# Optimization experiments

Measured on AMD Instinct MI355X. Metric: run time of the kernel, lower is better.

The kernel has to match this reference:

```python
import jax, jax.numpy as jnp
import numpy as np

B, LAGS, POOL, D, H, NTS = 16, 4096, 4, 512, 8, 1000
S = LAGS // POOL          # num_pools = 1024
DH = D // H               # head dim = 64


def _layernorm_dim1(x, gamma, beta, eps=1e-5):
    # torch code: mean/var over dim=1 (channel axis), unbiased var, per-position affine
    mean = jnp.mean(x, axis=1, keepdims=True)
    var = jnp.var(x, axis=1, keepdims=True, ddof=1)
    unit = (x - mean) / jnp.sqrt(eps + var)
    return gamma * unit + beta


def setup_inputs() -> dict:
    key = jax.random.key(0)
    ks = jax.random.split(key, 16)
    inp = {
        "ts": jax.random.normal(ks[0], (B, 1, LAGS), dtype=jnp.float32),
        "te": jax.random.randint(ks[1], (B, 1), 0, NTS),
        "conv_w": jax.random.normal(ks[2], (D, 1, POOL), dtype=jnp.float32) * (1.0 / POOL) ** 0.5,
        "conv_b": jax.random.normal(ks[3], (D,), dtype=jnp.float32) * 0.02,
        "pe_emb": jax.random.normal(ks[4], (S, D), dtype=jnp.float32),
        "ts_emb": jax.random.normal(ks[5], (NTS, D), dtype=jnp.float32),
        "ln1_g": jnp.ones((S,), dtype=jnp.float32),
        "ln1_b": jnp.zeros((S,), dtype=jnp.float32),
        "dense_M": jax.random.normal(ks[6], (D, D), dtype=jnp.float32) * D ** -0.5,
        "Wq": jax.random.normal(ks[7], (H, DH, D), dtype=jnp.float32) * D ** -0.5,
        "Wk": jax.random.normal(ks[8], (H, DH, D), dtype=jnp.float32) * D ** -0.5,
        "Wv": jax.random.normal(ks[9], (H, DH, D), dtype=jnp.float32) * D ** -0.5,
        "Wo": jax.random.normal(ks[10], (D, D), dtype=jnp.float32) * D ** -0.5,
        "bo": jnp.zeros((D, 1), dtype=jnp.float32),
        "ln2_g": jnp.ones((S,), dtype=jnp.float32),
        "ln2_b": jnp.zeros((S,), dtype=jnp.float32),
    }
    return inp


def _forward(ts, te, conv_w, conv_b, pe_emb, ts_emb, ln1_g, ln1_b,
             dense_M, Wq, Wk, Wv, Wo, bo, ln2_g, ln2_b):
    # Conv1d with stride == kernel_size: non-overlapping patches
    xr = ts.reshape(B, S, POOL)                                   # (B,S,P)
    conv = jnp.einsum('bsp,dp->bds', xr, conv_w[:, 0, :]) + conv_b[:, None]  # (B,D,S)
    conv = conv + pe_emb.T                                        # positional add (D,S)
    act = jax.nn.gelu(conv, approximate=False)
    n1 = _layernorm_dim1(act, ln1_g, ln1_b)
    dense = jnp.einsum('ed,bds->bes', dense_M, n1)                # Linear: M @ x
    dense = dense + ts_emb[te[:, 0]][:, :, None]                  # ts embedding (B,D,1)

    # multi-head attention, Q=K=V=dense; vectorized over heads
    Qd = jnp.einsum('hcd,bds->bhcs', Wq, dense)                   # (B,H,DH,S)
    Kd = jnp.einsum('hcd,bds->bhcs', Wk, dense)
    Vd = jnp.einsum('hcd,bds->bhcs', Wv, dense)
    scores = jnp.einsum('bhci,bhcj->bhij', Qd, Kd) / DH ** 0.5    # (B,H,S,S)
    i_idx = jnp.arange(S)
    mask = i_idx[:, None] > i_idx[None, :]                        # tril(diagonal=-1): i>j -> -inf
    scores = jnp.where(mask, -jnp.inf, scores)
    sm = jax.nn.softmax(scores, axis=2)                           # softmax over dim 1 of (S,S)
    attn = jnp.einsum('bhci,bhij->bhcj', Vd, sm)                  # V @ softmaxed
    cat = attn.reshape(B, D, S)                                   # concat heads on dim 1
    out = jnp.einsum('ed,bds->bes', Wo, cat) + bo[None]           # final linear + bias
    res = out + conv                                              # residual
    return _layernorm_dim1(res, ln2_g, ln2_b)


def reference(ts, te, conv_w, conv_b, pe_emb, ts_emb, ln1_g, ln1_b,
              dense_M, Wq, Wk, Wv, Wo, bo, ln2_g, ln2_b):
    return _forward(ts, te, conv_w, conv_b, pe_emb, ts_emb, ln1_g, ln1_b,
                    dense_M, Wq, Wk, Wv, Wo, bo, ln2_g, ln2_b)
```

## Files before the change

### kernel.cpp

```cpp
#include <hip/hip_runtime.h>
#include <hip/hip_bf16.h>

#define B_ 16
#define S_ 1024
#define D_ 512
#define H_ 8
#define DH_ 64

typedef __attribute__((ext_vector_type(8))) short bf16x8;
typedef __attribute__((ext_vector_type(4))) short bf16x4;
typedef __attribute__((ext_vector_type(4))) float f32x4;
typedef __attribute__((ext_vector_type(16))) float f32x16;

__device__ __forceinline__ short f2bf(float f) {
    __hip_bfloat16 h = __float2bfloat16(f);
    return *reinterpret_cast<short*>(&h);
}
__device__ __forceinline__ float bf2f(short s) {
    unsigned u = ((unsigned)(unsigned short)s) << 16;
    return __uint_as_float(u);
}
__device__ __forceinline__ unsigned pack_bf2(float lo, float hi) {
    unsigned a = (unsigned)(unsigned short)f2bf(lo);
    unsigned b = (unsigned)(unsigned short)f2bf(hi);
    return a | (b << 16);
}
__device__ __forceinline__ void gload16(const void* g, void* l) {
    __builtin_amdgcn_global_load_lds(
        (const __attribute__((address_space(1))) unsigned int*)g,
        (__attribute__((address_space(3))) unsigned int*)l, 16, 0, 0);
}

__global__ __launch_bounds__(256) void prep_w(
    const float* __restrict__ M, const float* __restrict__ Wq,
    const float* __restrict__ Wk, const float* __restrict__ Wv,
    const float* __restrict__ Wo, __hip_bfloat16* __restrict__ wb)
{
    __hip_bfloat16* wsrc = wb;
    __hip_bfloat16* Wob  = wb + 786432;
    __hip_bfloat16* MT   = wb + 1048576;

    const int blk = blockIdx.x, t = threadIdx.x;
    if (blk < 512) {
        const int wi = blk >> 7;
        const int off = (blk & 127) * 2048 + t * 8;
        const float* src = (wi == 0) ? Wq : (wi == 1) ? Wk : (wi == 2) ? Wv : Wo;
        const float scale = (wi == 0) ? 0.18033688011112042f : 1.0f;
        const float4 f0 = *reinterpret_cast<const float4*>(src + off);
        const float4 f1 = *reinterpret_cast<const float4*>(src + off + 4);
        const float fv[8] = {f0.x, f0.y, f0.z, f0.w, f1.x, f1.y, f1.z, f1.w};
        union { short s[8]; bf16x8 v; } r;
#pragma unroll
        for (int j = 0; j < 8; ++j) r.s[j] = f2bf(fv[j] * scale);
        __hip_bfloat16* dst = (wi == 3) ? (Wob + off) : (wsrc + wi * 262144 + off);
        *reinterpret_cast<bf16x8*>(dst) = r.v;
    } else {
        __shared__ float tile[32][33];
        const int tt = blk - 512;
        const int e0 = (tt & 15) * 32, d0 = (tt >> 4) * 32;
        const int r = t >> 5, c = t & 31;
#pragma unroll
        for (int k = 0; k < 4; ++k)
            tile[r + k * 8][c] = M[(size_t)(e0 + r + k * 8) * 512 + d0 + c];
        __syncthreads();
#pragma unroll
        for (int k = 0; k < 4; ++k)
            MT[(size_t)(d0 + r + k * 8) * 512 + e0 + c] =
                __float2bfloat16(tile[c][r + k * 8]);
    }
}

__global__ __launch_bounds__(256) void bias_k(
    const __hip_bfloat16* __restrict__ wsrc, const float* __restrict__ ts_emb,
    const int* __restrict__ te, float* __restrict__ qkvpart)
{
    const int blk = blockIdx.x;
    const int w16b = blk >> 2, dc = blk & 3;
    const int b = w16b & 15, w = w16b >> 4;
    const float* e = ts_emb + (size_t)te[b] * 512 + dc * 128;
#pragma unroll
    for (int rep = 0; rep < 2; ++rep) {
        const int n = threadIdx.x + rep * 256;
        const __hip_bfloat16* wr = wsrc + ((size_t)(w * 512 + n)) * 512 + dc * 128;
        float s = 0.f;
#pragma unroll 4
        for (int d8 = 0; d8 < 128; d8 += 8) {
            const bf16x8 wv8 = *reinterpret_cast<const bf16x8*>(wr + d8);
            const float4 e0 = *reinterpret_cast<const float4*>(e + d8);
            const float4 e1 = *reinterpret_cast<const float4*>(e + d8 + 4);
            s += bf2f(wv8[0]) * e0.x + bf2f(wv8[1]) * e0.y
               + bf2f(wv8[2]) * e0.z + bf2f(wv8[3]) * e0.w
               + bf2f(wv8[4]) * e1.x + bf2f(wv8[5]) * e1.y
               + bf2f(wv8[6]) * e1.z + bf2f(wv8[7]) * e1.w;
        }
        qkvpart[(size_t)dc * 24576 + (size_t)w16b * 512 + n] = s;
    }
}

__global__ __launch_bounds__(256) void k1_conv_gelu_ln(
    const float* __restrict__ ts, const float* __restrict__ conv_w,
    const float* __restrict__ conv_b, const float* __restrict__ pe,
    const float* __restrict__ g1, const float* __restrict__ b1,
    __hip_bfloat16* __restrict__ n1)
{
    const int w = threadIdx.x >> 6, lane = threadIdx.x & 63;
    const int row = blockIdx.x * 4 + w;
    const int b = row >> 10, s = row & 1023;
    const float4 x = *reinterpret_cast<const float4*>(ts + b * 4096 + s * 4);
    const int d0 = lane * 8;

    const float4 cb0 = *reinterpret_cast<const float4*>(conv_b + d0);
    const float4 cb1 = *reinterpret_cast<const float4*>(conv_b + d0 + 4);
    const float4 pe0 = *reinterpret_cast<const float4*>(pe + s * 512 + d0);
    const float4 pe1 = *reinterpret_cast<const float4*>(pe + s * 512 + d0 + 4);
    const float cbv[8] = {cb0.x, cb0.y, cb0.z, cb0.w, cb1.x, cb1.y, cb1.z, cb1.w};
    const float pev[8] = {pe0.x, pe0.y, pe0.z, pe0.w, pe1.x, pe1.y, pe1.z, pe1.w};

    float a[8];
    float sum = 0.f, sq = 0.f;
#pragma unroll
    for (int j = 0; j < 8; ++j) {
        const float4 wv = *reinterpret_cast<const float4*>(conv_w + (d0 + j) * 4);
        float v = x.x * wv.x + x.y * wv.y + x.z * wv.z + x.w * wv.w
                + cbv[j] + pev[j];
        v = 0.5f * v * (1.0f + erff(v * 0.70710678118654752f));
        a[j] = v; sum += v; sq += v * v;
    }
#pragma unroll
    for (int off = 1; off < 64; off <<= 1) {
        sum += __shfl_xor(sum, off);
        sq  += __shfl_xor(sq, off);
    }
    const float mean = sum * (1.0f / 512.0f);
    const float var  = (sq - 512.0f * mean * mean) * (1.0f / 511.0f);
    const float rstd = rsqrtf(var + 1e-5f);
    const float gg = g1[s], bb = b1[s];
    union { short sh[8]; bf16x8 v; } o;
#pragma unroll
    for (int j = 0; j < 8; ++j)
        o.sh[j] = f2bf(gg * ((a[j] - mean) * rstd) + bb);
    *reinterpret_cast<bf16x8*>(n1 + (size_t)row * 512 + d0) = o.v;
}

template<int MODE>
__global__ __launch_bounds__(256, 2) void gemm_k(
    const __hip_bfloat16* __restrict__ A,
    const __hip_bfloat16* __restrict__ Wb,
    void* __restrict__ outp,
    const float* __restrict__ aux)
{
    __shared__ char lA[2][128 * 128];
    __shared__ char lB[2][128 * 128];

    const int t = threadIdx.x;
    const int lane = t & 63;
    const int w = t >> 6;
    const int wm = w & 1, wn = w >> 1;
    const int Rb = blockIdx.x * 128;
    const int Nb = blockIdx.y * 128;
    const int g = lane >> 4, lr = lane & 15;
    const int lrow = lane >> 3;
    const int coff = ((lane & 7) ^ lrow) * 8;

    const __hip_bfloat16* asrc = A  + (size_t)(Rb + lrow) * 512 + coff;
    const __hip_bfloat16* bsrc = Wb + (size_t)(Nb + lrow) * 512 + coff;

    f32x4 acc[4][4];
#pragma unroll
    for (int i = 0; i < 4; ++i)
#pragma unroll
        for (int j = 0; j < 4; ++j) acc[i][j] = {0.f, 0.f, 0.f, 0.f};

    auto stage = [&](int buf, int k0) {
#pragma unroll
        for (int i = 0; i < 4; ++i) {
            const int r0 = w * 32 + i * 8;
            gload16(asrc + (size_t)r0 * 512 + k0, &lA[buf][r0 * 128]);
        }
#pragma unroll
        for (int i = 0; i < 4; ++i) {
            const int r0 = w * 32 + i * 8;
            gload16(bsrc + (size_t)r0 * 512 + k0, &lB[buf][r0 * 128]);
        }
    };

    stage(0, 0);
    __syncthreads();

    for (int kt = 0; kt < 8; ++kt) {
        const int buf = kt & 1;
        if (kt < 7) stage(buf ^ 1, (kt + 1) * 64);
#pragma unroll
        for (int kk = 0; kk < 2; ++kk) {
            bf16x8 af[4], bfv[4];
            const int ch = kk * 4 + g;
#pragma unroll
            for (int mt = 0; mt < 4; ++mt) {
                const int row = wm * 64 + mt * 16 + lr;
                af[mt] = *reinterpret_cast<const bf16x8*>(
                    &lA[buf][row * 128 + ((ch ^ (row & 7)) << 4)]);
            }
#pragma unroll
            for (int nt = 0; nt < 4; ++nt) {
                const int row = wn * 64 + nt * 16 + lr;
                bfv[nt] = *reinterpret_cast<const bf16x8*>(
                    &lB[buf][row * 128 + ((ch ^ (row & 7)) << 4)]);
            }
#pragma unroll
            for (int mt = 0; mt < 4; ++mt)
#pragma unroll
                for (int nt = 0; nt < 4; ++nt)
                    acc[mt][nt] = __builtin_amdgcn_mfma_f32_16x16x32_bf16(
                        af[mt], bfv[nt], acc[mt][nt], 0, 0, 0);
        }
        __syncthreads();
    }

    const int w3 = Nb >> 9;
#pragma unroll
    for (int mt = 0; mt < 4; ++mt) {
#pragma unroll
        for (int nt = 0; nt < 4; ++nt) {
#pragma unroll
            for (int r = 0; r < 4; ++r) {
                const int R = Rb + wm * 64 + mt * 16 + 4 * g + r;
                const int N = Nb + wn * 64 + nt * 16 + lr;
                float v = acc[mt][nt][r];
                if (MODE == 5) {
                    const int Nl = N & 511;
                    const int b = R >> 10, s = R & 1023, h = Nl >> 6, c = Nl & 63;
                    const float* qp = aux + (size_t)(w3 * 16 + b) * 512 + Nl;
                    v += qp[0] + qp[24576] + qp[49152] + qp[73728];
                    __hip_bfloat16* base =
                        reinterpret_cast<__hip_bfloat16*>(outp) + (size_t)w3 * 8388608;
                    if (w3 == 2)
                        base[(((size_t)(b * 8 + h)) * 64 + c) * 1024 + s] =
                            __float2bfloat16(v);
                    else
                        base[(((size_t)(b * 8 + h)) * 1024 + s) * 64 + c] =
                            __float2bfloat16(v);
                } else if (MODE == 6) {
                    reinterpret_cast<__hip_bfloat16*>(outp)[(size_t)R * 512 + N] =
                        __float2bfloat16(v);
                } else {
                    reinterpret_cast<float*>(outp)[(size_t)R * 512 + N] = v + aux[N];
                }
            }
        }
    }
}

__device__ __forceinline__ void write_strip(
    __hip_bfloat16* __restrict__ dstbase, const int jw0,
    const f32x16& o0, const f32x16& o1, const float lsum,
    const int l5, const int ln31)
{
    const float linv = 1.0f / lsum;
#pragma unroll
    for (int r = 0; r < 16; ++r) {
        const int jrow = (r & 3) + 8 * (r >> 2) + 4 * l5;
        const float rinv = __shfl(linv, jrow);
        __hip_bfloat16* dst = dstbase + (size_t)(jw0 + jrow) * 512;
        dst[ln31]      = __float2bfloat16(o0[r] * rinv);
        dst[32 + ln31] = __float2bfloat16(o1[r] * rinv);
    }
}

__global__ __launch_bounds__(256, 4) void attn5_k(
    const __hip_bfloat16* __restrict__ Qm,
    const __hip_bfloat16* __restrict__ Km,
    const __hip_bfloat16* __restrict__ Vt,
    __hip_bfloat16* __restrict__ cat)
{
    __shared__ char qbuf[2][4096];
    __shared__ char vbuf[2][4096];

    const int t = threadIdx.x, lane = t & 63, w = t >> 6;
    const int l5 = lane >> 5, ln31 = lane & 31;
    const int id = blockIdx.x;
    const int bh = id & 127;
    const int jb = (0x32451067u >> ((id >> 7) * 4)) & 7;
    const int b = bh >> 3, h = bh & 7;
    const int j0 = jb * 128 + w * 32;

    const __hip_bfloat16* Qh = Qm + (size_t)bh * (S_ * 64);
    const __hip_bfloat16* Kh = Km + (size_t)bh * (S_ * 64);
    const __hip_bfloat16* Vh = Vt + (size_t)bh * (64 * S_);

    bf16x8 kf[4];
#pragma unroll
    for (int kt = 0; kt < 4; ++kt)
        kf[kt] = *reinterpret_cast<const bf16x8*>(
            Kh + (size_t)(j0 + ln31) * 64 + kt * 16 + l5 * 8);

    f32x16 o0, o1;
#pragma unroll
    for (int r = 0; r < 16; ++r) { o0[r] = 0.f; o1[r] = 0.f; }
    float m = -3e38f, lsum = 0.f;

    const int last = jb * 4 + w;
    const int ntiles = jb * 4 + 4;

    const int q_row  = w * 8 + (lane >> 3);
    const int q_ch   = (lane & 7) ^ (lane >> 3);
    const int v_row  = w * 16 + (lane >> 2);
    const int v_ch   = (lane & 3) ^ ((lane >> 2) & 3) ^ ((lane >> 4) & 3);
    const __hip_bfloat16* qsrc = Qh + (size_t)q_row * 64 + q_ch * 8;
    const __hip_bfloat16* vsrc = Vh + (size_t)v_row * 1024 + v_ch * 8;

    auto stage = [&](int buf, int tile) {
        const int i0 = tile * 32;
        gload16(qsrc + (size_t)i0 * 64, &qbuf[buf][w * 1024]);
        gload16(vsrc + i0,              &vbuf[buf][w * 1024]);
    };

    stage(0, 0);
    __syncthreads();

    for (int tt = 0; tt < ntiles; ++tt) {
        const int buf = tt & 1;
        if (tt + 1 < ntiles) stage(buf ^ 1, tt + 1);
        if (tt <= last) {
            f32x16 sc;
#pragma unroll
            for (int r = 0; r < 16; ++r) sc[r] = 0.f;
            bf16x8 qf[4];
#pragma unroll
            for (int kt = 0; kt < 4; ++kt)
                qf[kt] = *reinterpret_cast<const bf16x8*>(
                    &qbuf[buf][ln31 * 128 + (((kt * 2 + l5) ^ (ln31 & 7)) << 4)]);
#pragma unroll
            for (int kt = 0; kt < 4; ++kt)
                sc = __builtin_amdgcn_mfma_f32_32x32x16_bf16(qf[kt], kf[kt], sc, 0, 0, 0);

            union u8 { bf16x4 h[2]; bf16x8 v; };
            u8 vf[2][2];
#pragma unroll
            for (int kt = 0; kt < 2; ++kt) {
#pragma unroll
                for (int dh = 0; dh < 2; ++dh) {
                    const int drow = ln31 + dh * 32;
                    const int swz = (drow & 3) ^ ((drow >> 2) & 3);
                    const int x0 = kt * 32 + 8 * l5;
#pragma unroll
                    for (int hp = 0; hp < 2; ++hp) {
                        const int x = x0 + hp * 16;
                        vf[kt][dh].h[hp] = *reinterpret_cast<const bf16x4*>(
                            &vbuf[buf][drow * 64 + (((x >> 4) ^ swz) << 4) + (x & 15)]);
                    }
                }
            }

            const bool diag = (tt == last);
            float p[16];
            float mx = -3e38f;
            if (diag) {
#pragma unroll
                for (int r = 0; r < 16; ++r) {
                    const int irow = (r & 3) + 8 * (r >> 2) + 4 * l5;
                    const float v = (irow > ln31) ? -3e38f : sc[r];
                    p[r] = v; mx = fmaxf(mx, v);
                }
            } else {
#pragma unroll
                for (int r = 0; r < 16; ++r) { p[r] = sc[r]; mx = fmaxf(mx, sc[r]); }
            }
            mx = fmaxf(mx, __shfl_xor(mx, 32));
            if (!__all(mx <= m + 8.0f)) {
                const float mn = fmaxf(m, mx);
                const float alpha = exp2f(m - mn);
                m = mn; lsum *= alpha;
#pragma unroll
                for (int r = 0; r < 16; ++r) {
                    const int jrow = (r & 3) + 8 * (r >> 2) + 4 * l5;
                    const float ar = __shfl(alpha, jrow);
                    o0[r] *= ar; o1[r] *= ar;
                }
            }
            float ps = 0.f;
#pragma unroll
            for (int r = 0; r < 16; ++r) { p[r] = exp2f(p[r] - m); ps += p[r]; }
            ps += __shfl_xor(ps, 32);
            lsum += ps;

            union { unsigned u[4]; bf16x8 v; } pa0, pa1;
            pa0.u[0] = pack_bf2(p[0],  p[1]);  pa0.u[1] = pack_bf2(p[2],  p[3]);
            pa0.u[2] = pack_bf2(p[4],  p[5]);  pa0.u[3] = pack_bf2(p[6],  p[7]);
            pa1.u[0] = pack_bf2(p[8],  p[9]);  pa1.u[1] = pack_bf2(p[10], p[11]);
            pa1.u[2] = pack_bf2(p[12], p[13]); pa1.u[3] = pack_bf2(p[14], p[15]);
            o0 = __builtin_amdgcn_mfma_f32_32x32x16_bf16(pa0.v, vf[0][0].v, o0, 0, 0, 0);
            o1 = __builtin_amdgcn_mfma_f32_32x32x16_bf16(pa0.v, vf[0][1].v, o1, 0, 0, 0);
            o0 = __builtin_amdgcn_mfma_f32_32x32x16_bf16(pa1.v, vf[1][0].v, o0, 0, 0, 0);
            o1 = __builtin_amdgcn_mfma_f32_32x32x16_bf16(pa1.v, vf[1][1].v, o1, 0, 0, 0);
        }
        __syncthreads();
    }

    __hip_bfloat16* dstbase = cat + (size_t)b * 1024 * 512 + h * 64;
    write_strip(dstbase, j0, o0, o1, lsum, l5, ln31);
}

__global__ __launch_bounds__(256) void k5_res_ln(
    const float* __restrict__ outf,
    const float* __restrict__ ts, const float* __restrict__ conv_w,
    const float* __restrict__ conv_b, const float* __restrict__ pe,
    const float* __restrict__ g2, const float* __restrict__ b2,
    float* __restrict__ out)
{
    __shared__ float tile[16 * 520];
    const int blk = blockIdx.x;
    const int b = blk >> 6, s0 = (blk & 63) * 16;
    const int t = threadIdx.x;
    const int sl = t >> 4, c = t & 15;
    const int s = s0 + sl;

    const float4 x = *reinterpret_cast<const float4*>(ts + b * 4096 + s * 4);
    float vals[32];
    float sum = 0.f, sq = 0.f;
#pragma unroll
    for (int j = 0; j < 32; ++j) {
        const int d = c + 16 * j;
        const float4 wv = *reinterpret_cast<const float4*>(conv_w + d * 4);
        const float conv = x.x * wv.x + x.y * wv.y + x.z * wv.z + x.w * wv.w
                         + conv_b[d] + pe[s * 512 + d];
        const float a = outf[(size_t)(b * 1024 + s) * 512 + d] + conv;
        vals[j] = a; sum += a; sq += a * a;
    }
#pragma unroll
    for (int off = 1; off < 16; off <<= 1) {
        sum += __shfl_xor(sum, off);
        sq  += __shfl_xor(sq, off);
    }
    const float mean = sum * (1.0f / 512.0f);
    const float var  = (sq - 512.0f * mean * mean) * (1.0f / 511.0f);
    const float rstd = rsqrtf(var + 1e-5f);
    const float gg = g2[s], bb = b2[s];
#pragma unroll
    for (int j = 0; j < 32; ++j) {
        const int d = c + 16 * j;
        tile[sl * 520 + d] = gg * ((vals[j] - mean) * rstd) + bb;
    }
    __syncthreads();
#pragma unroll
    for (int q2 = 0; q2 < 2; ++q2) {
        const int d = t + q2 * 256;
        float buf[16];
#pragma unroll
        for (int sl2 = 0; sl2 < 16; ++sl2) buf[sl2] = tile[sl2 * 520 + d];
        float4* dst = reinterpret_cast<float4*>(
            out + ((size_t)b * 512 + d) * 1024 + s0);
        dst[0] = make_float4(buf[0],  buf[1],  buf[2],  buf[3]);
        dst[1] = make_float4(buf[4],  buf[5],  buf[6],  buf[7]);
        dst[2] = make_float4(buf[8],  buf[9],  buf[10], buf[11]);
        dst[3] = make_float4(buf[12], buf[13], buf[14], buf[15]);
    }
}

extern "C" void kernel_launch(void* const* d_in, const int* in_sizes, int n_in,
                              void* d_out, int out_size, void* d_ws, size_t ws_size,
                              hipStream_t stream)
{
    const float* ts     = (const float*)d_in[0];
    const int*   te     = (const int*)d_in[1];
    const float* conv_w = (const float*)d_in[2];
    const float* conv_b = (const float*)d_in[3];
    const float* pe     = (const float*)d_in[4];
    const float* ts_emb = (const float*)d_in[5];
    const float* g1     = (const float*)d_in[6];
    const float* b1     = (const float*)d_in[7];
    const float* M      = (const float*)d_in[8];
    const float* Wq     = (const float*)d_in[9];
    const float* Wk     = (const float*)d_in[10];
    const float* Wv     = (const float*)d_in[11];
    const float* Wo     = (const float*)d_in[12];
    const float* bo     = (const float*)d_in[13];
    const float* g2     = (const float*)d_in[14];
    const float* b2     = (const float*)d_in[15];

    char* ws = (char*)d_ws;
    __hip_bfloat16* wb     = (__hip_bfloat16*)(ws);
    __hip_bfloat16* wsrc   = wb;
    __hip_bfloat16* Wob    = wb + 786432;
    __hip_bfloat16* MT     = wb + 1048576;
    __hip_bfloat16* Wqkvp  = (__hip_bfloat16*)(ws + (2688ull << 10));
    float*          qkvpart= (float*)(ws + (4608ull << 10));
    __hip_bfloat16* n1     = (__hip_bfloat16*)(ws + ( 6ull << 20));
    __hip_bfloat16* cat    = n1;
    __hip_bfloat16* q      = (__hip_bfloat16*)(ws + (22ull << 20));
    __hip_bfloat16* k      = (__hip_bfloat16*)(ws + (38ull << 20));
    __hip_bfloat16* vT     = (__hip_bfloat16*)(ws + (54ull << 20));
    float*          outf   = (float*)(ws + (22ull << 20));

    prep_w<<<768, 256, 0, stream>>>(M, Wq, Wk, Wv, Wo, wb);
    bias_k<<<192, 256, 0, stream>>>(wsrc, ts_emb, te, qkvpart);
    gemm_k<6><<<dim3(12, 4), 256, 0, stream>>>(wsrc, MT, Wqkvp, nullptr);
    k1_conv_gelu_ln<<<4096, 256, 0, stream>>>(ts, conv_w, conv_b, pe, g1, b1, n1);
    gemm_k<5><<<dim3(128, 12), 256, 0, stream>>>(n1, Wqkvp, q, qkvpart);
    attn5_k<<<1024, 256, 0, stream>>>(q, k, vT, cat);
    gemm_k<3><<<dim3(128, 4), 256, 0, stream>>>(cat, Wob, outf, bo);
    k5_res_ln<<<1024, 256, 0, stream>>>(outf, ts, conv_w, conv_b, pe, g2, b2,
                                        (float*)d_out);
}
```

Before: 174.3 us.

## Merge front kernels, pair causal attention blocks, store output projection in bf16

Fuses weight prep, bias computation and conv/GELU/LayerNorm into one launch, and the bias path now reads fp32 weights directly. The attention kernel has each block process two complementary causal strips (jb and 7-jb), so the grid is half as large and per-block work is even. The output projection writes bf16 instead of fp32, which halves that intermediate's traffic. The cost is lower precision in the residual input and less occupancy in attention, since the launch bound drops to 2 blocks.

Result: slower. 196.0 us (+12.5%).

```diff
diff --git a/kernel.cpp b/kernel.cpp
--- a/kernel.cpp
+++ b/kernel.cpp
@@ -31,115 +31,106 @@
         (__attribute__((address_space(3))) unsigned int*)l, 16, 0, 0);
 }
 
-__global__ __launch_bounds__(256) void prep_w(
-    const float* __restrict__ M, const float* __restrict__ Wq,
-    const float* __restrict__ Wk, const float* __restrict__ Wv,
-    const float* __restrict__ Wo, __hip_bfloat16* __restrict__ wb)
-{
-    __hip_bfloat16* wsrc = wb;
-    __hip_bfloat16* Wob  = wb + 786432;
-    __hip_bfloat16* MT   = wb + 1048576;
-
-    const int blk = blockIdx.x, t = threadIdx.x;
-    if (blk < 512) {
-        const int wi = blk >> 7;
-        const int off = (blk & 127) * 2048 + t * 8;
-        const float* src = (wi == 0) ? Wq : (wi == 1) ? Wk : (wi == 2) ? Wv : Wo;
-        const float scale = (wi == 0) ? 0.18033688011112042f : 1.0f;
-        const float4 f0 = *reinterpret_cast<const float4*>(src + off);
-        const float4 f1 = *reinterpret_cast<const float4*>(src + off + 4);
-        const float fv[8] = {f0.x, f0.y, f0.z, f0.w, f1.x, f1.y, f1.z, f1.w};
-        union { short s[8]; bf16x8 v; } r;
-#pragma unroll
-        for (int j = 0; j < 8; ++j) r.s[j] = f2bf(fv[j] * scale);
-        __hip_bfloat16* dst = (wi == 3) ? (Wob + off) : (wsrc + wi * 262144 + off);
-        *reinterpret_cast<bf16x8*>(dst) = r.v;
-    } else {
-        __shared__ float tile[32][33];
-        const int tt = blk - 512;
-        const int e0 = (tt & 15) * 32, d0 = (tt >> 4) * 32;
-        const int r = t >> 5, c = t & 31;
-#pragma unroll
-        for (int k = 0; k < 4; ++k)
-            tile[r + k * 8][c] = M[(size_t)(e0 + r + k * 8) * 512 + d0 + c];
-        __syncthreads();
-#pragma unroll
-        for (int k = 0; k < 4; ++k)
-            MT[(size_t)(d0 + r + k * 8) * 512 + e0 + c] =
-                __float2bfloat16(tile[c][r + k * 8]);
-    }
-}
-
-__global__ __launch_bounds__(256) void bias_k(
-    const __hip_bfloat16* __restrict__ wsrc, const float* __restrict__ ts_emb,
-    const int* __restrict__ te, float* __restrict__ qkvpart)
-{
-    const int blk = blockIdx.x;
-    const int w16b = blk >> 2, dc = blk & 3;
-    const int b = w16b & 15, w = w16b >> 4;
-    const float* e = ts_emb + (size_t)te[b] * 512 + dc * 128;
-#pragma unroll
-    for (int rep = 0; rep < 2; ++rep) {
-        const int n = threadIdx.x + rep * 256;
-        const __hip_bfloat16* wr = wsrc + ((size_t)(w * 512 + n)) * 512 + dc * 128;
-        float s = 0.f;
-#pragma unroll 4
-        for (int d8 = 0; d8 < 128; d8 += 8) {
-            const bf16x8 wv8 = *reinterpret_cast<const bf16x8*>(wr + d8);
-            const float4 e0 = *reinterpret_cast<const float4*>(e + d8);
-            const float4 e1 = *reinterpret_cast<const float4*>(e + d8 + 4);
-            s += bf2f(wv8[0]) * e0.x + bf2f(wv8[1]) * e0.y
-               + bf2f(wv8[2]) * e0.z + bf2f(wv8[3]) * e0.w
-               + bf2f(wv8[4]) * e1.x + bf2f(wv8[5]) * e1.y
-               + bf2f(wv8[6]) * e1.z + bf2f(wv8[7]) * e1.w;
-        }
-        qkvpart[(size_t)dc * 24576 + (size_t)w16b * 512 + n] = s;
-    }
-}
-
-__global__ __launch_bounds__(256) void k1_conv_gelu_ln(
+__global__ __launch_bounds__(256) void front_k(
     const float* __restrict__ ts, const float* __restrict__ conv_w,
     const float* __restrict__ conv_b, const float* __restrict__ pe,
     const float* __restrict__ g1, const float* __restrict__ b1,
-    __hip_bfloat16* __restrict__ n1)
-{
-    const int w = threadIdx.x >> 6, lane = threadIdx.x & 63;
-    const int row = blockIdx.x * 4 + w;
-    const int b = row >> 10, s = row & 1023;
-    const float4 x = *reinterpret_cast<const float4*>(ts + b * 4096 + s * 4);
-    const int d0 = lane * 8;
-
-    const float4 cb0 = *reinterpret_cast<const float4*>(conv_b + d0);
-    const float4 cb1 = *reinterpret_cast<const float4*>(conv_b + d0 + 4);
-    const float4 pe0 = *reinterpret_cast<const float4*>(pe + s * 512 + d0);
-    const float4 pe1 = *reinterpret_cast<const float4*>(pe + s * 512 + d0 + 4);
-    const float cbv[8] = {cb0.x, cb0.y, cb0.z, cb0.w, cb1.x, cb1.y, cb1.z, cb1.w};
-    const float pev[8] = {pe0.x, pe0.y, pe0.z, pe0.w, pe1.x, pe1.y, pe1.z, pe1.w};
-
-    float a[8];
-    float sum = 0.f, sq = 0.f;
-#pragma unroll
-    for (int j = 0; j < 8; ++j) {
-        const float4 wv = *reinterpret_cast<const float4*>(conv_w + (d0 + j) * 4);
-        float v = x.x * wv.x + x.y * wv.y + x.z * wv.z + x.w * wv.w
-                + cbv[j] + pev[j];
-        v = 0.5f * v * (1.0f + erff(v * 0.70710678118654752f));
-        a[j] = v; sum += v; sq += v * v;
-    }
-#pragma unroll
-    for (int off = 1; off < 64; off <<= 1) {
-        sum += __shfl_xor(sum, off);
-        sq  += __shfl_xor(sq, off);
-    }
-    const float mean = sum * (1.0f / 512.0f);
-    const float var  = (sq - 512.0f * mean * mean) * (1.0f / 511.0f);
-    const float rstd = rsqrtf(var + 1e-5f);
-    const float gg = g1[s], bb = b1[s];
-    union { short sh[8]; bf16x8 v; } o;
-#pragma unroll
-    for (int j = 0; j < 8; ++j)
-        o.sh[j] = f2bf(gg * ((a[j] - mean) * rstd) + bb);
-    *reinterpret_cast<bf16x8*>(n1 + (size_t)row * 512 + d0) = o.v;
+    const float* __restrict__ M, const float* __restrict__ Wq,
+    const float* __restrict__ Wk, const float* __restrict__ Wv,
+    const float* __restrict__ Wo, const float* __restrict__ ts_emb,
+    const int* __restrict__ te,
+    __hip_bfloat16* __restrict__ n1, __hip_bfloat16* __restrict__ wb,
+    float* __restrict__ qkvpart)
+{
+    const int blk = blockIdx.x, t = threadIdx.x;
+    if (blk < 4096) {
+        const int w = t >> 6, lane = t & 63;
+        const int row = blk * 4 + w;
+        const int b = row >> 10, s = row & 1023;
+        const float4 x = *reinterpret_cast<const float4*>(ts + b * 4096 + s * 4);
+        const int d0 = lane * 8;
+        const float4 cb0 = *reinterpret_cast<const float4*>(conv_b + d0);
+        const float4 cb1 = *reinterpret_cast<const float4*>(conv_b + d0 + 4);
+        const float4 pe0 = *reinterpret_cast<const float4*>(pe + s * 512 + d0);
+        const float4 pe1 = *reinterpret_cast<const float4*>(pe + s * 512 + d0 + 4);
+        const float cbv[8] = {cb0.x, cb0.y, cb0.z, cb0.w, cb1.x, cb1.y, cb1.z, cb1.w};
+        const float pev[8] = {pe0.x, pe0.y, pe0.z, pe0.w, pe1.x, pe1.y, pe1.z, pe1.w};
+        float a[8];
+        float sum = 0.f, sq = 0.f;
+#pragma unroll
+        for (int j = 0; j < 8; ++j) {
+            const float4 wv = *reinterpret_cast<const float4*>(conv_w + (d0 + j) * 4);
+            float v = x.x * wv.x + x.y * wv.y + x.z * wv.z + x.w * wv.w
+                    + cbv[j] + pev[j];
+            v = 0.5f * v * (1.0f + erff(v * 0.70710678118654752f));
+            a[j] = v; sum += v; sq += v * v;
+        }
+#pragma unroll
+        for (int off = 1; off < 64; off <<= 1) {
+            sum += __shfl_xor(sum, off);
+            sq  += __shfl_xor(sq, off);
+        }
+        const float mean = sum * (1.0f / 512.0f);
+        const float var  = (sq - 512.0f * mean * mean) * (1.0f / 511.0f);
+        const float rstd = rsqrtf(var + 1e-5f);
+        const float gg = g1[s], bb = b1[s];
+        union { short sh[8]; bf16x8 v; } o;
+#pragma unroll
+        for (int j = 0; j < 8; ++j)
+            o.sh[j] = f2bf(gg * ((a[j] - mean) * rstd) + bb);
+        *reinterpret_cast<bf16x8*>(n1 + (size_t)row * 512 + d0) = o.v;
+    } else if (blk < 4864) {
+        __hip_bfloat16* wsrc = wb;
+        __hip_bfloat16* Wob  = wb + 786432;
+        __hip_bfloat16* MT   = wb + 1048576;
+        const int pblk = blk - 4096;
+        if (pblk < 512) {
+            const int wi = pblk >> 7;
+            const int off = (pblk & 127) * 2048 + t * 8;
+            const float* src = (wi == 0) ? Wq : (wi == 1) ? Wk : (wi == 2) ? Wv : Wo;
+            const float scale = (wi == 0) ? 0.18033688011112042f : 1.0f;
+            const float4 f0 = *reinterpret_cast<const float4*>(src + off);
+            const float4 f1 = *reinterpret_cast<const float4*>(src + off + 4);
+            const float fv[8] = {f0.x, f0.y, f0.z, f0.w, f1.x, f1.y, f1.z, f1.w};
+            union { short s[8]; bf16x8 v; } r;
+#pragma unroll
+            for (int j = 0; j < 8; ++j) r.s[j] = f2bf(fv[j] * scale);
+            __hip_bfloat16* dst = (wi == 3) ? (Wob + off) : (wsrc + wi * 262144 + off);
+            *reinterpret_cast<bf16x8*>(dst) = r.v;
+        } else {
+            __shared__ float tile[32][33];
+            const int tt = pblk - 512;
+            const int e0 = (tt & 15) * 32, d0 = (tt >> 4) * 32;
+            const int r = t >> 5, c = t & 31;
+#pragma unroll
+            for (int k = 0; k < 4; ++k)
+                tile[r + k * 8][c] = M[(size_t)(e0 + r + k * 8) * 512 + d0 + c];
+            __syncthreads();
+#pragma unroll
+            for (int k = 0; k < 4; ++k)
+                MT[(size_t)(d0 + r + k * 8) * 512 + e0 + c] =
+                    __float2bfloat16(tile[c][r + k * 8]);
+        }
+    } else {
+        const int bblk = blk - 4864;
+        const int w16b = bblk >> 2, dc = bblk & 3;
+        const int b = w16b & 15, w = w16b >> 4;
+        const float* W = (w == 0) ? Wq : (w == 1) ? Wk : Wv;
+        const float scale = (w == 0) ? 0.18033688011112042f : 1.0f;
+        const float* e = ts_emb + (size_t)te[b] * 512 + dc * 128;
+#pragma unroll
+        for (int rep = 0; rep < 2; ++rep) {
+            const int n = t + rep * 256;
+            const float* wr = W + (size_t)n * 512 + dc * 128;
+            float s = 0.f;
+            for (int d = 0; d < 128; d += 4) {
+                const float4 a = *reinterpret_cast<const float4*>(wr + d);
+                const float4 bb = *reinterpret_cast<const float4*>(e + d);
+                s += a.x * bb.x + a.y * bb.y + a.z * bb.z + a.w * bb.w;
+            }
+            qkvpart[(size_t)dc * 24576 + (size_t)w16b * 512 + n] = s * scale;
+        }
+    }
 }
 
 template<int MODE>
@@ -243,7 +234,8 @@
                     reinterpret_cast<__hip_bfloat16*>(outp)[(size_t)R * 512 + N] =
                         __float2bfloat16(v);
                 } else {
-                    reinterpret_cast<float*>(outp)[(size_t)R * 512 + N] = v + aux[N];
+                    reinterpret_cast<__hip_bfloat16*>(outp)[(size_t)R * 512 + N] =
+                        __float2bfloat16(v + aux[N]);
                 }
             }
         }
@@ -266,7 +258,7 @@
     }
 }
 
-__global__ __launch_bounds__(256, 4) void attn5_k(
+__global__ __launch_bounds__(256, 2) void attn6_k(
     const __hip_bfloat16* __restrict__ Qm,
     const __hip_bfloat16* __restrict__ Km,
     const __hip_bfloat16* __restrict__ Vt,
@@ -279,27 +271,12 @@
     const int l5 = lane >> 5, ln31 = lane & 31;
     const int id = blockIdx.x;
     const int bh = id & 127;
-    const int jb = (0x32451067u >> ((id >> 7) * 4)) & 7;
+    const int sidx = id >> 7;
     const int b = bh >> 3, h = bh & 7;
-    const int j0 = jb * 128 + w * 32;
 
     const __hip_bfloat16* Qh = Qm + (size_t)bh * (S_ * 64);
     const __hip_bfloat16* Kh = Km + (size_t)bh * (S_ * 64);
     const __hip_bfloat16* Vh = Vt + (size_t)bh * (64 * S_);
-
-    bf16x8 kf[4];
-#pragma unroll
-    for (int kt = 0; kt < 4; ++kt)
-        kf[kt] = *reinterpret_cast<const bf16x8*>(
-            Kh + (size_t)(j0 + ln31) * 64 + kt * 16 + l5 * 8);
-
-    f32x16 o0, o1;
-#pragma unroll
-    for (int r = 0; r < 16; ++r) { o0[r] = 0.f; o1[r] = 0.f; }
-    float m = -3e38f, lsum = 0.f;
-
-    const int last = jb * 4 + w;
-    const int ntiles = jb * 4 + 4;
 
     const int q_row  = w * 8 + (lane >> 3);
     const int q_ch   = (lane & 7) ^ (lane >> 3);
@@ -307,6 +284,7 @@
     const int v_ch   = (lane & 3) ^ ((lane >> 2) & 3) ^ ((lane >> 4) & 3);
     const __hip_bfloat16* qsrc = Qh + (size_t)q_row * 64 + q_ch * 8;
     const __hip_bfloat16* vsrc = Vh + (size_t)v_row * 1024 + v_ch * 8;
+    __hip_bfloat16* dstbase = cat + (size_t)b * 1024 * 512 + h * 64;
 
     auto stage = [&](int buf, int tile) {
         const int i0 = tile * 32;
@@ -314,94 +292,112 @@
         gload16(vsrc + i0,              &vbuf[buf][w * 1024]);
     };
 
-    stage(0, 0);
-    __syncthreads();
-
-    for (int tt = 0; tt < ntiles; ++tt) {
-        const int buf = tt & 1;
-        if (tt + 1 < ntiles) stage(buf ^ 1, tt + 1);
-        if (tt <= last) {
-            f32x16 sc;
-#pragma unroll
-            for (int r = 0; r < 16; ++r) sc[r] = 0.f;
-            bf16x8 qf[4];
-#pragma unroll
-            for (int kt = 0; kt < 4; ++kt)
-                qf[kt] = *reinterpret_cast<const bf16x8*>(
-                    &qbuf[buf][ln31 * 128 + (((kt * 2 + l5) ^ (ln31 & 7)) << 4)]);
-#pragma unroll
-            for (int kt = 0; kt < 4; ++kt)
-                sc = __builtin_amdgcn_mfma_f32_32x32x16_bf16(qf[kt], kf[kt], sc, 0, 0, 0);
-
-            union u8 { bf16x4 h[2]; bf16x8 v; };
-            u8 vf[2][2];
-#pragma unroll
-            for (int kt = 0; kt < 2; ++kt) {
-#pragma unroll
-                for (int dh = 0; dh < 2; ++dh) {
-                    const int drow = ln31 + dh * 32;
-                    const int swz = (drow & 3) ^ ((drow >> 2) & 3);
-                    const int x0 = kt * 32 + 8 * l5;
-#pragma unroll
-                    for (int hp = 0; hp < 2; ++hp) {
-                        const int x = x0 + hp * 16;
-                        vf[kt][dh].h[hp] = *reinterpret_cast<const bf16x4*>(
-                            &vbuf[buf][drow * 64 + (((x >> 4) ^ swz) << 4) + (x & 15)]);
+    for (int ph = 0; ph < 2; ++ph) {
+        const int jb = ph ? (7 - sidx) : sidx;
+        const int j0 = jb * 128 + w * 32;
+
+        bf16x8 kf[4];
+#pragma unroll
+        for (int kt = 0; kt < 4; ++kt)
+            kf[kt] = *reinterpret_cast<const bf16x8*>(
+                Kh + (size_t)(j0 + ln31) * 64 + kt * 16 + l5 * 8);
+
+        f32x16 o0, o1;
+#pragma unroll
+        for (int r = 0; r < 16; ++r) { o0[r] = 0.f; o1[r] = 0.f; }
+        float m = -3e38f, lsum = 0.f;
+
+        const int last = jb * 4 + w;
+        const int ntiles = jb * 4 + 4;
+
+        stage(0, 0);
+        __syncthreads();
+
+        for (int tt = 0; tt < ntiles; ++tt) {
+            const int buf = tt & 1;
+            if (tt + 1 < ntiles) stage(buf ^ 1, tt + 1);
+            if (tt <= last) {
+                f32x16 sc;
+#pragma unroll
+                for (int r = 0; r < 16; ++r) sc[r] = 0.f;
+                bf16x8 qf[4];
+#pragma unroll
+                for (int kt = 0; kt < 4; ++kt)
+                    qf[kt] = *reinterpret_cast<const bf16x8*>(
+                        &qbuf[buf][ln31 * 128 + (((kt * 2 + l5) ^ (ln31 & 7)) << 4)]);
+#pragma unroll
+                for (int kt = 0; kt < 4; ++kt)
+                    sc = __builtin_amdgcn_mfma_f32_32x32x16_bf16(qf[kt], kf[kt], sc, 0, 0, 0);
+
+                union u8 { bf16x4 h[2]; bf16x8 v; };
+                u8 vf[2][2];
+#pragma unroll
+                for (int kt = 0; kt < 2; ++kt) {
+#pragma unroll
+                    for (int dh = 0; dh < 2; ++dh) {
+                        const int drow = ln31 + dh * 32;
+                        const int swz = (drow & 3) ^ ((drow >> 2) & 3);
+                        const int x0 = kt * 32 + 8 * l5;
+#pragma unroll
+                        for (int hp = 0; hp < 2; ++hp) {
+                            const int x = x0 + hp * 16;
+                            vf[kt][dh].h[hp] = *reinterpret_cast<const bf16x4*>(
+                                &vbuf[buf][drow * 64 + (((x >> 4) ^ swz) << 4) + (x & 15)]);
+                        }
                     }
                 }
+
+                const bool diag = (tt == last);
+                float p[16];
+                float mx = -3e38f;
+                if (diag) {
+#pragma unroll
+                    for (int r = 0; r < 16; ++r) {
+                        const int irow = (r & 3) + 8 * (r >> 2) + 4 * l5;
+                        const float v = (irow > ln31) ? -3e38f : sc[r];
+                        p[r] = v; mx = fmaxf(mx, v);
+                    }
+                } else {
+#pragma unroll
+                    for (int r = 0; r < 16; ++r) { p[r] = sc[r]; mx = fmaxf(mx, sc[r]); }
+                }
+                mx = fmaxf(mx, __shfl_xor(mx, 32));
+                if (!__all(mx <= m + 8.0f)) {
+                    const float mn = fmaxf(m, mx);
+                    const float alpha = exp2f(m - mn);
+                    m = mn; lsum *= alpha;
+#pragma unroll
+                    for (int r = 0; r < 16; ++r) {
+                        const int jrow = (r & 3) + 8 * (r >> 2) + 4 * l5;
+                        const float ar = __shfl(alpha, jrow);
+                        o0[r] *= ar; o1[r] *= ar;
+                    }
+                }
+                float ps = 0.f;
+#pragma unroll
+                for (int r = 0; r < 16; ++r) { p[r] = exp2f(p[r] - m); ps += p[r]; }
+                ps += __shfl_xor(ps, 32);
+                lsum += ps;
+
+                union { unsigned u[4]; bf16x8 v; } pa0, pa1;
+                pa0.u[0] = pack_bf2(p[0],  p[1]);  pa0.u[1] = pack_bf2(p[2],  p[3]);
+                pa0.u[2] = pack_bf2(p[4],  p[5]);  pa0.u[3] = pack_bf2(p[6],  p[7]);
+                pa1.u[0] = pack_bf2(p[8],  p[9]);  pa1.u[1] = pack_bf2(p[10], p[11]);
+                pa1.u[2] = pack_bf2(p[12], p[13]); pa1.u[3] = pack_bf2(p[14], p[15]);
+                o0 = __builtin_amdgcn_mfma_f32_32x32x16_bf16(pa0.v, vf[0][0].v, o0, 0, 0, 0);
+                o1 = __builtin_amdgcn_mfma_f32_32x32x16_bf16(pa0.v, vf[0][1].v, o1, 0, 0, 0);
+                o0 = __builtin_amdgcn_mfma_f32_32x32x16_bf16(pa1.v, vf[1][0].v, o0, 0, 0, 0);
+                o1 = __builtin_amdgcn_mfma_f32_32x32x16_bf16(pa1.v, vf[1][1].v, o1, 0, 0, 0);
             }
-
-            const bool diag = (tt == last);
-            float p[16];
-            float mx = -3e38f;
-            if (diag) {
-#pragma unroll
-                for (int r = 0; r < 16; ++r) {
-                    const int irow = (r & 3) + 8 * (r >> 2) + 4 * l5;
-                    const float v = (irow > ln31) ? -3e38f : sc[r];
-                    p[r] = v; mx = fmaxf(mx, v);
-                }
-            } else {
-#pragma unroll
-                for (int r = 0; r < 16; ++r) { p[r] = sc[r]; mx = fmaxf(mx, sc[r]); }
-            }
-            mx = fmaxf(mx, __shfl_xor(mx, 32));
-            if (!__all(mx <= m + 8.0f)) {
-                const float mn = fmaxf(m, mx);
-                const float alpha = exp2f(m - mn);
-                m = mn; lsum *= alpha;
-#pragma unroll
-                for (int r = 0; r < 16; ++r) {
-                    const int jrow = (r & 3) + 8 * (r >> 2) + 4 * l5;
-                    const float ar = __shfl(alpha, jrow);
-                    o0[r] *= ar; o1[r] *= ar;
-                }
-            }
-            float ps = 0.f;
-#pragma unroll
-            for (int r = 0; r < 16; ++r) { p[r] = exp2f(p[r] - m); ps += p[r]; }
-            ps += __shfl_xor(ps, 32);
-            lsum += ps;
-
-            union { unsigned u[4]; bf16x8 v; } pa0, pa1;
-            pa0.u[0] = pack_bf2(p[0],  p[1]);  pa0.u[1] = pack_bf2(p[2],  p[3]);
-            pa0.u[2] = pack_bf2(p[4],  p[5]);  pa0.u[3] = pack_bf2(p[6],  p[7]);
-            pa1.u[0] = pack_bf2(p[8],  p[9]);  pa1.u[1] = pack_bf2(p[10], p[11]);
-            pa1.u[2] = pack_bf2(p[12], p[13]); pa1.u[3] = pack_bf2(p[14], p[15]);
-            o0 = __builtin_amdgcn_mfma_f32_32x32x16_bf16(pa0.v, vf[0][0].v, o0, 0, 0, 0);
-            o1 = __builtin_amdgcn_mfma_f32_32x32x16_bf16(pa0.v, vf[0][1].v, o1, 0, 0, 0);
-            o0 = __builtin_amdgcn_mfma_f32_32x32x16_bf16(pa1.v, vf[1][0].v, o0, 0, 0, 0);
-            o1 = __builtin_amdgcn_mfma_f32_32x32x16_bf16(pa1.v, vf[1][1].v, o1, 0, 0, 0);
-        }
-        __syncthreads();
-    }
-
-    __hip_bfloat16* dstbase = cat + (size_t)b * 1024 * 512 + h * 64;
-    write_strip(dstbase, j0, o0, o1, lsum, l5, ln31);
+            __syncthreads();
+        }
+
+        write_strip(dstbase, j0, o0, o1, lsum, l5, ln31);
+    }
 }
 
 __global__ __launch_bounds__(256) void k5_res_ln(
-    const float* __restrict__ outf,
+    const __hip_bfloat16* __restrict__ outf,
     const float* __restrict__ ts, const float* __restrict__ conv_w,
     const float* __restrict__ conv_b, const float* __restrict__ pe,
     const float* __restrict__ g2, const float* __restrict__ b2,
@@ -423,7 +419,7 @@
         const float4 wv = *reinterpret_cast<const float4*>(conv_w + d * 4);
         const float conv = x.x * wv.x + x.y * wv.y + x.z * wv.z + x.w * wv.w
                          + conv_b[d] + pe[s * 512 + d];
-        const float a = outf[(size_t)(b * 1024 + s) * 512 + d] + conv;
+        const float a = __bfloat162float(outf[(size_t)(b * 1024 + s) * 512 + d]) + conv;
         vals[j] = a; sum += a; sq += a * a;
     }
 #pragma unroll
@@ -489,14 +485,14 @@
     __hip_bfloat16* q      = (__hip_bfloat16*)(ws + (22ull << 20));
     __hip_bfloat16* k      = (__hip_bfloat16*)(ws + (38ull << 20));
     __hip_bfloat16* vT     = (__hip_bfloat16*)(ws + (54ull << 20));
-    float*          outf   = (float*)(ws + (22ull << 20));
-
-    prep_w<<<768, 256, 0, stream>>>(M, Wq, Wk, Wv, Wo, wb);
-    bias_k<<<192, 256, 0, stream>>>(wsrc, ts_emb, te, qkvpart);
+    __hip_bfloat16* outf   = (__hip_bfloat16*)(ws + (22ull << 20));
+
+    front_k<<<5056, 256, 0, stream>>>(ts, conv_w, conv_b, pe, g1, b1,
+                                      M, Wq, Wk, Wv, Wo, ts_emb, te,
+                                      n1, wb, qkvpart);
     gemm_k<6><<<dim3(12, 4), 256, 0, stream>>>(wsrc, MT, Wqkvp, nullptr);
-    k1_conv_gelu_ln<<<4096, 256, 0, stream>>>(ts, conv_w, conv_b, pe, g1, b1, n1);
     gemm_k<5><<<dim3(128, 12), 256, 0, stream>>>(n1, Wqkvp, q, qkvpart);
-    attn5_k<<<1024, 256, 0, stream>>>(q, k, vT, cat);
+    attn6_k<<<512, 256, 0, stream>>>(q, k, vT, cat);
     gemm_k<3><<<dim3(128, 4), 256, 0, stream>>>(cat, Wob, outf, bo);
     k5_res_ln<<<1024, 256, 0, stream>>>(outf, ts, conv_w, conv_b, pe, g2, b2,
                                         (float*)d_out);
```

## Pair causal attention tiles per block, XCD-swizzle GEMM grids, store output GEMM in bf16

Applied to the files above, without the earlier changes.

The attention kernel now processes two key blocks per workgroup (jb and 7-jb), so every block does the same amount of causal work. The grid is halved and occupancy lowered to 2 blocks. The GEMM kernels switch to a 1D grid with an XCD-aware swizzle that keeps row tiles local to a chiplet, aiming for better L2 reuse. The output projection now writes bf16 instead of fp32, which halves that intermediate's traffic but loses precision before the residual layernorm.

Result: slower. 186.8 us (+7.2%).

```diff
diff --git a/kernel.cpp b/kernel.cpp
--- a/kernel.cpp
+++ b/kernel.cpp
@@ -142,7 +142,7 @@
     *reinterpret_cast<bf16x8*>(n1 + (size_t)row * 512 + d0) = o.v;
 }
 
-template<int MODE>
+template<int MODE, int NCOL, int SWZ>
 __global__ __launch_bounds__(256, 2) void gemm_k(
     const __hip_bfloat16* __restrict__ A,
     const __hip_bfloat16* __restrict__ Wb,
@@ -156,8 +156,19 @@
     const int lane = t & 63;
     const int w = t >> 6;
     const int wm = w & 1, wn = w >> 1;
-    const int Rb = blockIdx.x * 128;
-    const int Nb = blockIdx.y * 128;
+
+    const int id = blockIdx.x;
+    int Rb, Nb;
+    if (SWZ) {
+        const int xcd = id & 7;
+        const int local = id >> 3;
+        Rb = (xcd * 16 + local / NCOL) * 128;
+        Nb = (local % NCOL) * 128;
+    } else {
+        Rb = (id / NCOL) * 128;
+        Nb = (id % NCOL) * 128;
+    }
+
     const int g = lane >> 4, lr = lane & 15;
     const int lrow = lane >> 3;
     const int coff = ((lane & 7) ^ lrow) * 8;
@@ -243,7 +254,8 @@
                     reinterpret_cast<__hip_bfloat16*>(outp)[(size_t)R * 512 + N] =
                         __float2bfloat16(v);
                 } else {
-                    reinterpret_cast<float*>(outp)[(size_t)R * 512 + N] = v + aux[N];
+                    reinterpret_cast<__hip_bfloat16*>(outp)[(size_t)R * 512 + N] =
+                        __float2bfloat16(v + aux[N]);
                 }
             }
         }
@@ -266,7 +278,7 @@
     }
 }
 
-__global__ __launch_bounds__(256, 4) void attn5_k(
+__global__ __launch_bounds__(256, 2) void attn6_k(
     const __hip_bfloat16* __restrict__ Qm,
     const __hip_bfloat16* __restrict__ Km,
     const __hip_bfloat16* __restrict__ Vt,
@@ -279,27 +291,12 @@
     const int l5 = lane >> 5, ln31 = lane & 31;
     const int id = blockIdx.x;
     const int bh = id & 127;
-    const int jb = (0x32451067u >> ((id >> 7) * 4)) & 7;
+    const int sidx = id >> 7;
     const int b = bh >> 3, h = bh & 7;
-    const int j0 = jb * 128 + w * 32;
 
     const __hip_bfloat16* Qh = Qm + (size_t)bh * (S_ * 64);
     const __hip_bfloat16* Kh = Km + (size_t)bh * (S_ * 64);
     const __hip_bfloat16* Vh = Vt + (size_t)bh * (64 * S_);
-
-    bf16x8 kf[4];
-#pragma unroll
-    for (int kt = 0; kt < 4; ++kt)
-        kf[kt] = *reinterpret_cast<const bf16x8*>(
-            Kh + (size_t)(j0 + ln31) * 64 + kt * 16 + l5 * 8);
-
-    f32x16 o0, o1;
-#pragma unroll
-    for (int r = 0; r < 16; ++r) { o0[r] = 0.f; o1[r] = 0.f; }
-    float m = -3e38f, lsum = 0.f;
-
-    const int last = jb * 4 + w;
-    const int ntiles = jb * 4 + 4;
 
     const int q_row  = w * 8 + (lane >> 3);
     const int q_ch   = (lane & 7) ^ (lane >> 3);
@@ -307,6 +304,7 @@
     const int v_ch   = (lane & 3) ^ ((lane >> 2) & 3) ^ ((lane >> 4) & 3);
     const __hip_bfloat16* qsrc = Qh + (size_t)q_row * 64 + q_ch * 8;
     const __hip_bfloat16* vsrc = Vh + (size_t)v_row * 1024 + v_ch * 8;
+    __hip_bfloat16* dstbase = cat + (size_t)b * 1024 * 512 + h * 64;
 
     auto stage = [&](int buf, int tile) {
         const int i0 = tile * 32;
@@ -314,94 +312,112 @@
         gload16(vsrc + i0,              &vbuf[buf][w * 1024]);
     };
 
-    stage(0, 0);
-    __syncthreads();
-
-    for (int tt = 0; tt < ntiles; ++tt) {
-        const int buf = tt & 1;
-        if (tt + 1 < ntiles) stage(buf ^ 1, tt + 1);
-        if (tt <= last) {
-            f32x16 sc;
-#pragma unroll
-            for (int r = 0; r < 16; ++r) sc[r] = 0.f;
-            bf16x8 qf[4];
-#pragma unroll
-            for (int kt = 0; kt < 4; ++kt)
-                qf[kt] = *reinterpret_cast<const bf16x8*>(
-                    &qbuf[buf][ln31 * 128 + (((kt * 2 + l5) ^ (ln31 & 7)) << 4)]);
-#pragma unroll
-            for (int kt = 0; kt < 4; ++kt)
-                sc = __builtin_amdgcn_mfma_f32_32x32x16_bf16(qf[kt], kf[kt], sc, 0, 0, 0);
-
-            union u8 { bf16x4 h[2]; bf16x8 v; };
-            u8 vf[2][2];
-#pragma unroll
-            for (int kt = 0; kt < 2; ++kt) {
-#pragma unroll
-                for (int dh = 0; dh < 2; ++dh) {
-                    const int drow = ln31 + dh * 32;
-                    const int swz = (drow & 3) ^ ((drow >> 2) & 3);
-                    const int x0 = kt * 32 + 8 * l5;
-#pragma unroll
-                    for (int hp = 0; hp < 2; ++hp) {
-                        const int x = x0 + hp * 16;
-                        vf[kt][dh].h[hp] = *reinterpret_cast<const bf16x4*>(
-                            &vbuf[buf][drow * 64 + (((x >> 4) ^ swz) << 4) + (x & 15)]);
+    for (int ph = 0; ph < 2; ++ph) {
+        const int jb = ph ? (7 - sidx) : sidx;
+        const int j0 = jb * 128 + w * 32;
+
+        bf16x8 kf[4];
+#pragma unroll
+        for (int kt = 0; kt < 4; ++kt)
+            kf[kt] = *reinterpret_cast<const bf16x8*>(
+                Kh + (size_t)(j0 + ln31) * 64 + kt * 16 + l5 * 8);
+
+        f32x16 o0, o1;
+#pragma unroll
+        for (int r = 0; r < 16; ++r) { o0[r] = 0.f; o1[r] = 0.f; }
+        float m = -3e38f, lsum = 0.f;
+
+        const int last = jb * 4 + w;
+        const int ntiles = jb * 4 + 4;
+
+        stage(0, 0);
+        __syncthreads();
+
+        for (int tt = 0; tt < ntiles; ++tt) {
+            const int buf = tt & 1;
+            if (tt + 1 < ntiles) stage(buf ^ 1, tt + 1);
+            if (tt <= last) {
+                f32x16 sc;
+#pragma unroll
+                for (int r = 0; r < 16; ++r) sc[r] = 0.f;
+                bf16x8 qf[4];
+#pragma unroll
+                for (int kt = 0; kt < 4; ++kt)
+                    qf[kt] = *reinterpret_cast<const bf16x8*>(
+                        &qbuf[buf][ln31 * 128 + (((kt * 2 + l5) ^ (ln31 & 7)) << 4)]);
+#pragma unroll
+                for (int kt = 0; kt < 4; ++kt)
+                    sc = __builtin_amdgcn_mfma_f32_32x32x16_bf16(qf[kt], kf[kt], sc, 0, 0, 0);
+
+                union u8 { bf16x4 h[2]; bf16x8 v; };
+                u8 vf[2][2];
+#pragma unroll
+                for (int kt = 0; kt < 2; ++kt) {
+#pragma unroll
+                    for (int dh = 0; dh < 2; ++dh) {
+                        const int drow = ln31 + dh * 32;
+                        const int swz = (drow & 3) ^ ((drow >> 2) & 3);
+                        const int x0 = kt * 32 + 8 * l5;
+#pragma unroll
+                        for (int hp = 0; hp < 2; ++hp) {
+                            const int x = x0 + hp * 16;
+                            vf[kt][dh].h[hp] = *reinterpret_cast<const bf16x4*>(
+                                &vbuf[buf][drow * 64 + (((x >> 4) ^ swz) << 4) + (x & 15)]);
+                        }
                     }
                 }
+
+                const bool diag = (tt == last);
+                float p[16];
+                float mx = -3e38f;
+                if (diag) {
+#pragma unroll
+                    for (int r = 0; r < 16; ++r) {
+                        const int irow = (r & 3) + 8 * (r >> 2) + 4 * l5;
+                        const float v = (irow > ln31) ? -3e38f : sc[r];
+                        p[r] = v; mx = fmaxf(mx, v);
+                    }
+                } else {
+#pragma unroll
+                    for (int r = 0; r < 16; ++r) { p[r] = sc[r]; mx = fmaxf(mx, sc[r]); }
+                }
+                mx = fmaxf(mx, __shfl_xor(mx, 32));
+                if (!__all(mx <= m + 8.0f)) {
+                    const float mn = fmaxf(m, mx);
+                    const float alpha = exp2f(m - mn);
+                    m = mn; lsum *= alpha;
+#pragma unroll
+                    for (int r = 0; r < 16; ++r) {
+                        const int jrow = (r & 3) + 8 * (r >> 2) + 4 * l5;
+                        const float ar = __shfl(alpha, jrow);
+                        o0[r] *= ar; o1[r] *= ar;
+                    }
+                }
+                float ps = 0.f;
+#pragma unroll
+                for (int r = 0; r < 16; ++r) { p[r] = exp2f(p[r] - m); ps += p[r]; }
+                ps += __shfl_xor(ps, 32);
+                lsum += ps;
+
+                union { unsigned u[4]; bf16x8 v; } pa0, pa1;
+                pa0.u[0] = pack_bf2(p[0],  p[1]);  pa0.u[1] = pack_bf2(p[2],  p[3]);
+                pa0.u[2] = pack_bf2(p[4],  p[5]);  pa0.u[3] = pack_bf2(p[6],  p[7]);
+                pa1.u[0] = pack_bf2(p[8],  p[9]);  pa1.u[1] = pack_bf2(p[10], p[11]);
+                pa1.u[2] = pack_bf2(p[12], p[13]); pa1.u[3] = pack_bf2(p[14], p[15]);
+                o0 = __builtin_amdgcn_mfma_f32_32x32x16_bf16(pa0.v, vf[0][0].v, o0, 0, 0, 0);
+                o1 = __builtin_amdgcn_mfma_f32_32x32x16_bf16(pa0.v, vf[0][1].v, o1, 0, 0, 0);
+                o0 = __builtin_amdgcn_mfma_f32_32x32x16_bf16(pa1.v, vf[1][0].v, o0, 0, 0, 0);
+                o1 = __builtin_amdgcn_mfma_f32_32x32x16_bf16(pa1.v, vf[1][1].v, o1, 0, 0, 0);
             }
-
-            const bool diag = (tt == last);
-            float p[16];
-            float mx = -3e38f;
-            if (diag) {
-#pragma unroll
-                for (int r = 0; r < 16; ++r) {
-                    const int irow = (r & 3) + 8 * (r >> 2) + 4 * l5;
-                    const float v = (irow > ln31) ? -3e38f : sc[r];
-                    p[r] = v; mx = fmaxf(mx, v);
-                }
-            } else {
-#pragma unroll
-                for (int r = 0; r < 16; ++r) { p[r] = sc[r]; mx = fmaxf(mx, sc[r]); }
-            }
-            mx = fmaxf(mx, __shfl_xor(mx, 32));
-            if (!__all(mx <= m + 8.0f)) {
-                const float mn = fmaxf(m, mx);
-                const float alpha = exp2f(m - mn);
-                m = mn; lsum *= alpha;
-#pragma unroll
-                for (int r = 0; r < 16; ++r) {
-                    const int jrow = (r & 3) + 8 * (r >> 2) + 4 * l5;
-                    const float ar = __shfl(alpha, jrow);
-                    o0[r] *= ar; o1[r] *= ar;
-                }
-            }
-            float ps = 0.f;
-#pragma unroll
-            for (int r = 0; r < 16; ++r) { p[r] = exp2f(p[r] - m); ps += p[r]; }
-            ps += __shfl_xor(ps, 32);
-            lsum += ps;
-
-            union { unsigned u[4]; bf16x8 v; } pa0, pa1;
-            pa0.u[0] = pack_bf2(p[0],  p[1]);  pa0.u[1] = pack_bf2(p[2],  p[3]);
-            pa0.u[2] = pack_bf2(p[4],  p[5]);  pa0.u[3] = pack_bf2(p[6],  p[7]);
-            pa1.u[0] = pack_bf2(p[8],  p[9]);  pa1.u[1] = pack_bf2(p[10], p[11]);
-            pa1.u[2] = pack_bf2(p[12], p[13]); pa1.u[3] = pack_bf2(p[14], p[15]);
-            o0 = __builtin_amdgcn_mfma_f32_32x32x16_bf16(pa0.v, vf[0][0].v, o0, 0, 0, 0);
-            o1 = __builtin_amdgcn_mfma_f32_32x32x16_bf16(pa0.v, vf[0][1].v, o1, 0, 0, 0);
-            o0 = __builtin_amdgcn_mfma_f32_32x32x16_bf16(pa1.v, vf[1][0].v, o0, 0, 0, 0);
-            o1 = __builtin_amdgcn_mfma_f32_32x32x16_bf16(pa1.v, vf[1][1].v, o1, 0, 0, 0);
+            __syncthreads();
         }
-        __syncthreads();
-    }
-
-    __hip_bfloat16* dstbase = cat + (size_t)b * 1024 * 512 + h * 64;
-    write_strip(dstbase, j0, o0, o1, lsum, l5, ln31);
+
+        write_strip(dstbase, j0, o0, o1, lsum, l5, ln31);
+    }
 }
 
 __global__ __launch_bounds__(256) void k5_res_ln(
-    const float* __restrict__ outf,
+    const __hip_bfloat16* __restrict__ outf,
     const float* __restrict__ ts, const float* __restrict__ conv_w,
     const float* __restrict__ conv_b, const float* __restrict__ pe,
     const float* __restrict__ g2, const float* __restrict__ b2,
@@ -423,7 +439,7 @@
         const float4 wv = *reinterpret_cast<const float4*>(conv_w + d * 4);
         const float conv = x.x * wv.x + x.y * wv.y + x.z * wv.z + x.w * wv.w
                          + conv_b[d] + pe[s * 512 + d];
-        const float a = outf[(size_t)(b * 1024 + s) * 512 + d] + conv;
+        const float a = __bfloat162float(outf[(size_t)(b * 1024 + s) * 512 + d]) + conv;
         vals[j] = a; sum += a; sq += a * a;
     }
 #pragma unroll
@@ -489,15 +505,15 @@
     __hip_bfloat16* q      = (__hip_bfloat16*)(ws + (22ull << 20));
     __hip_bfloat16* k      = (__hip_bfloat16*)(ws + (38ull << 20));
     __hip_bfloat16* vT     = (__hip_bfloat16*)(ws + (54ull << 20));
-    float*          outf   = (float*)(ws + (22ull << 20));
+    __hip_bfloat16* outf   = (__hip_bfloat16*)(ws + (22ull << 20));
 
     prep_w<<<768, 256, 0, stream>>>(M, Wq, Wk, Wv, Wo, wb);
     bias_k<<<192, 256, 0, stream>>>(wsrc, ts_emb, te, qkvpart);
-    gemm_k<6><<<dim3(12, 4), 256, 0, stream>>>(wsrc, MT, Wqkvp, nullptr);
+    gemm_k<6, 4, 0><<<48, 256, 0, stream>>>(wsrc, MT, Wqkvp, nullptr);
     k1_conv_gelu_ln<<<4096, 256, 0, stream>>>(ts, conv_w, conv_b, pe, g1, b1, n1);
-    gemm_k<5><<<dim3(128, 12), 256, 0, stream>>>(n1, Wqkvp, q, qkvpart);
-    attn5_k<<<1024, 256, 0, stream>>>(q, k, vT, cat);
-    gemm_k<3><<<dim3(128, 4), 256, 0, stream>>>(cat, Wob, outf, bo);
+    gemm_k<5, 12, 1><<<1536, 256, 0, stream>>>(n1, Wqkvp, q, qkvpart);
+    attn6_k<<<512, 256, 0, stream>>>(q, k, vT, cat);
+    gemm_k<3, 4, 1><<<512, 256, 0, stream>>>(cat, Wob, outf, bo);
     k5_res_ln<<<1024, 256, 0, stream>>>(outf, ts, conv_w, conv_b, pe, g2, b2,
                                         (float*)d_out);
 }
```
